# Performance work log

Measured on AMD Instinct MI355X. Metric: run time of the kernel, lower is better.

The kernel has to match this reference:

```python
import jax, jax.numpy as jnp
import numpy as np
import math

DIM = 1024
NUMHEADS = 16
HEAD_DIM = DIM // NUMHEADS
B, N = 4, 1024


def setup_inputs() -> dict:
    key = jax.random.key(0)
    ks = jax.random.split(key, 12)
    x = jax.random.normal(ks[0], (B, N, DIM), dtype=jnp.float32)
    decaymask = jax.random.uniform(ks[1], (NUMHEADS, N, N), dtype=jnp.float32)
    s = 1.0 / math.sqrt(DIM)
    wq = jax.random.normal(ks[2], (DIM, DIM), dtype=jnp.float32) * s
    bq = jnp.zeros((DIM,), dtype=jnp.float32)
    wk = jax.random.normal(ks[3], (DIM, DIM), dtype=jnp.float32) * s
    bk = jnp.zeros((DIM,), dtype=jnp.float32)
    wv = jax.random.normal(ks[4], (DIM, DIM), dtype=jnp.float32) * s
    bv = jnp.zeros((DIM,), dtype=jnp.float32)
    wo = jax.random.normal(ks[5], (DIM, DIM), dtype=jnp.float32) * s
    bo = jnp.zeros((DIM,), dtype=jnp.float32)
    return {"x": x, "decaymask": decaymask, "wq": wq, "bq": bq, "wk": wk,
            "bk": bk, "wv": wv, "bv": bv, "wo": wo, "bo": bo}


def reference(x, decaymask, wq, bq, wk, bk, wv, bv, wo, bo):
    Bx, Nx, D = x.shape
    # projections (torch Linear: x @ W^T + b)
    q = x @ wq.T + bq
    k = x @ wk.T + bk
    v = x @ wv.T + bv
    # [B, H, N, Hd]
    q = q.reshape(Bx, Nx, NUMHEADS, HEAD_DIM).transpose(0, 2, 1, 3)
    k = k.reshape(Bx, Nx, NUMHEADS, HEAD_DIM).transpose(0, 2, 1, 3)
    v = v.reshape(Bx, Nx, NUMHEADS, HEAD_DIM).transpose(0, 2, 1, 3)
    scores = jnp.einsum('bhqd,bhkd->bhqk', q, k) / math.sqrt(HEAD_DIM)
    scores = scores * decaymask[None]  # multiplicative decay mask before softmax
    attn = jax.nn.softmax(scores, axis=-1)
    out = jnp.einsum('bhqk,bhkd->bhqd', attn, v)
    out = out.transpose(0, 2, 1, 3).reshape(Bx, Nx, D)
    return out @ wo.T + bo
```

## Files before the change

kernel.cpp:

```cpp
#include <hip/hip_runtime.h>
#include <hip/hip_bf16.h>
#include <math.h>

typedef __bf16 bf16;
typedef __bf16 bf16x8 __attribute__((ext_vector_type(8)));
typedef __bf16 bf16x4 __attribute__((ext_vector_type(4)));
typedef float f32x4 __attribute__((ext_vector_type(4)));
typedef unsigned short u16;
typedef u16 u16x8 __attribute__((ext_vector_type(8)));

#define SEQ 1024
#define DIMSZ 1024
#define NHEADS 16
#define HEADDIM 64
#define BATCH 4
#define MTOK (BATCH * SEQ)

#define QSCALE 0.180336880f

typedef __attribute__((address_space(1))) const unsigned char gas_u8;
typedef __attribute__((address_space(3))) unsigned char las_u8;
__device__ __forceinline__ void gload16(const void* g, void* l) {
    __builtin_amdgcn_global_load_lds((const gas_u8*)g, (las_u8*)l, 16, 0, 0);
}

__device__ __forceinline__ void cvt_store(const float4 v, bf16* dst, int e0, float scale) {
    int row = e0 >> 10, col = e0 & 1023;
    int col2 = (col & ~63) | (col & 7) | (((((col >> 3) & 7) ^ (row & 7))) << 3);
    bf16x4 o;
    o[0] = (bf16)(v.x * scale);
    o[1] = (bf16)(v.y * scale);
    o[2] = (bf16)(v.z * scale);
    o[3] = (bf16)(v.w * scale);
    *reinterpret_cast<bf16x4*>(&dst[(size_t)row * 1024 + col2]) = o;
}

__global__ void cvt_all(const float4* __restrict__ x,
                        const float4* __restrict__ wq, const float4* __restrict__ wk,
                        const float4* __restrict__ wv, const float4* __restrict__ wo,
                        bf16* __restrict__ xb, bf16* __restrict__ wqkvb,
                        bf16* __restrict__ wob) {
    int i = blockIdx.x * blockDim.x + threadIdx.x;
    if (i < 1048576) {
        cvt_store(x[i], xb, i << 2, 1.f);
    } else {
        int li = i - 1048576;
        int mat = li >> 18, lj = li & 262143;
        const float4* s = (mat == 0) ? wq : (mat == 1) ? wk : (mat == 2) ? wv : wo;
        bf16* d = (mat < 3) ? (wqkvb + (size_t)mat * 1024 * 1024) : wob;
        cvt_store(s[lj], d, lj << 2, (mat == 0) ? QSCALE : 1.f);
    }
}

__device__ __forceinline__ bf16x8 fragswz(const bf16* base, int row, int kb) {
    return *reinterpret_cast<const bf16x8*>(
        reinterpret_cast<const char*>(base) + row * 128 + (kb ^ ((row & 7) << 4)));
}

#define LDT 72
__device__ __forceinline__ bf16x8 ldsfrag72(const bf16* base, int row0, int k0, int lane) {
    return *reinterpret_cast<const bf16x8*>(base + (row0 + (lane & 15)) * LDT + k0 + ((lane >> 4) << 3));
}

template <int WN, int OUT_F32>
__global__ __launch_bounds__(256) void gemm_glds(
    const bf16* __restrict__ A, const bf16* __restrict__ Bm,
    const float* __restrict__ b0, const float* __restrict__ b1, const float* __restrict__ b2,
    float s0, void* __restrict__ Cv, int M, int N, int K)
{
    __shared__ __align__(16) bf16 As[128 * 64];
    __shared__ __align__(16) bf16 Bs[WN * 32 * 64];

    const int BN = WN * 32;
    const int nbn = N / BN;
    const int wrk = (blockIdx.x & 7) * ((int)gridDim.x >> 3) + (blockIdx.x >> 3);
    const int bm = wrk / nbn, bn = wrk % nbn;
    const int m0 = bm << 7, n0 = bn * BN;
    const int tid = threadIdx.x, lane = tid & 63, wid = tid >> 6;
    const int wr = wid >> 1, wc = wid & 1;
    const int lq = lane & 15, g = lane >> 4;

    f32x4 acc[4][WN];
    #pragma unroll
    for (int m = 0; m < 4; ++m)
        #pragma unroll
        for (int n = 0; n < WN; ++n)
            acc[m][n] = (f32x4){0.f, 0.f, 0.f, 0.f};

    for (int kt = 0; kt < K; kt += 64) {
        #pragma unroll
        for (int i = 0; i < 4; ++i) {
            int rb = wid * 32 + i * 8;
            gload16(&A[(size_t)(m0 + rb + (lane >> 3)) * K + kt + ((lane & 7) << 3)],
                    &As[rb * 64]);
        }
        #pragma unroll
        for (int i = 0; i < WN; ++i) {
            int rb = wid * (WN * 8) + i * 8;
            gload16(&Bm[(size_t)(n0 + rb + (lane >> 3)) * K + kt + ((lane & 7) << 3)],
                    &Bs[rb * 64]);
        }
        __syncthreads();

        bf16x8 af[4][2], bfr[WN][2];
        #pragma unroll
        for (int m = 0; m < 4; ++m)
            #pragma unroll
            for (int h2 = 0; h2 < 2; ++h2)
                af[m][h2] = fragswz(As, wr * 64 + m * 16 + lq, h2 * 64 + g * 16);
        #pragma unroll
        for (int n = 0; n < WN; ++n)
            #pragma unroll
            for (int h2 = 0; h2 < 2; ++h2)
                bfr[n][h2] = fragswz(Bs, wc * (WN * 16) + n * 16 + lq, h2 * 64 + g * 16);

        #pragma unroll
        for (int m = 0; m < 4; ++m)
            #pragma unroll
            for (int n = 0; n < WN; ++n)
                #pragma unroll
                for (int h2 = 0; h2 < 2; ++h2)
                    acc[m][n] = __builtin_amdgcn_mfma_f32_16x16x32_bf16(
                        af[m][h2], bfr[n][h2], acc[m][n], 0, 0, 0);
        __syncthreads();
    }

    const int seg = n0 >> 10;
    const float* bp = (seg == 0) ? b0 : ((seg == 1) ? b1 : b2);
    const float bsc = (seg == 0) ? s0 : 1.f;

    #pragma unroll
    for (int m = 0; m < 4; ++m) {
        #pragma unroll
        for (int n = 0; n < WN; ++n) {
            int rbase = m0 + wr * 64 + m * 16 + (g << 2);
            int col = n0 + wc * (WN * 16) + n * 16 + lq;
            float bv = bp[col - (seg << 10)] * bsc;
            #pragma unroll
            for (int r = 0; r < 4; ++r) {
                float v = acc[m][n][r] + bv;
                if (OUT_F32)
                    ((float*)Cv)[(size_t)(rbase + r) * N + col] = v;
                else
                    ((bf16*)Cv)[(size_t)(rbase + r) * N + col] = (bf16)v;
            }
        }
    }
}

struct KVRegs { bf16x8 k0, k1; u16x8 v0, v1; };

__device__ __forceinline__ void issue_loads(KVRegs& r, const bf16* qkv, int brow,
                                            int koff, int voff, int tid) {
    const int rK = tid >> 3, o8 = (tid & 7) << 3;
    r.k0 = *reinterpret_cast<const bf16x8*>(&qkv[(size_t)(brow + rK) * 3072 + koff + o8]);
    r.k1 = *reinterpret_cast<const bf16x8*>(&qkv[(size_t)(brow + rK + 32) * 3072 + koff + o8]);
    const int rV = rK << 1;
    r.v0 = *reinterpret_cast<const u16x8*>(&qkv[(size_t)(brow + rV) * 3072 + voff + o8]);
    r.v1 = *reinterpret_cast<const u16x8*>(&qkv[(size_t)(brow + rV + 1) * 3072 + voff + o8]);
}

__device__ __forceinline__ void write_stage(const KVRegs& r, bf16* Kb, bf16* Vb, int tid) {
    const int rK = tid >> 3, o = tid & 7, o8 = o << 3;
    *reinterpret_cast<bf16x8*>(&Kb[rK * LDT + o8]) = r.k0;
    *reinterpret_cast<bf16x8*>(&Kb[(rK + 32) * LDT + o8]) = r.k1;
    const int rV = rK << 1;
    char* vb = reinterpret_cast<char*>(Vb);
    #pragma unroll
    for (int j = 0; j < 8; ++j) {
        int d = o8 + j;
        int byteo = (d * 144 + rV * 2) ^ (o << 4);
        unsigned int w = (unsigned int)r.v0[j] | ((unsigned int)r.v1[j] << 16);
        *reinterpret_cast<unsigned int*>(vb + byteo) = w;
    }
}

__device__ __forceinline__ void compute_stage(
    const bf16* Kb, const bf16* Vb, bf16* Psw,
    const float4 (&mreg)[4], const bf16x8 (&aqb)[2],
    f32x4& lacc, f32x4 (&oacc)[4], int lane)
{
    const int lq = lane & 15, g = lane >> 4;
    f32x4 sacc[4];
    #pragma unroll
    for (int ct = 0; ct < 4; ++ct) sacc[ct] = (f32x4){0.f, 0.f, 0.f, 0.f};
    #pragma unroll
    for (int ct = 0; ct < 4; ++ct)
        #pragma unroll
        for (int h2 = 0; h2 < 2; ++h2)
            sacc[ct] = __builtin_amdgcn_mfma_f32_16x16x32_bf16(
                ldsfrag72(Kb, ct * 16, h2 * 32, lane), aqb[h2], sacc[ct], 0, 0, 0);

    #pragma unroll
    for (int ct = 0; ct < 4; ++ct) {
        float p0 = __builtin_exp2f(sacc[ct][0] * mreg[ct].x);
        float p1 = __builtin_exp2f(sacc[ct][1] * mreg[ct].y);
        float p2 = __builtin_exp2f(sacc[ct][2] * mreg[ct].z);
        float p3 = __builtin_exp2f(sacc[ct][3] * mreg[ct].w);
        lacc[0] += p0; lacc[1] += p1; lacc[2] += p2; lacc[3] += p3;
        bf16x4 pbv;
        pbv[0] = (bf16)p0; pbv[1] = (bf16)p1; pbv[2] = (bf16)p2; pbv[3] = (bf16)p3;
        *reinterpret_cast<bf16x4*>(&Psw[lq * LDT + ct * 16 + (g << 2)]) = pbv;
    }

    const char* vb = reinterpret_cast<const char*>(Vb);
    #pragma unroll
    for (int ot = 0; ot < 4; ++ot) {
        #pragma unroll
        for (int h2 = 0; h2 < 2; ++h2) {
            int d = ot * 16 + lq;
            int byteo = (d * 144 + (h2 * 32 + g * 8) * 2) ^ (((d >> 3) & 7) << 4);
            bf16x8 vf = *reinterpret_cast<const bf16x8*>(vb + byteo);
            bf16x8 pf = *reinterpret_cast<const bf16x8*>(&Psw[lq * LDT + h2 * 32 + g * 8]);
            oacc[ot] = __builtin_amdgcn_mfma_f32_16x16x32_bf16(vf, pf, oacc[ot], 0, 0, 0);
        }
    }
}

__global__ __launch_bounds__(256) void attn_kernel(
    const bf16* __restrict__ qkv, const float* __restrict__ mask, bf16* __restrict__ Og)
{
    __shared__ __align__(16) bf16 Kbuf[2][64 * LDT];
    __shared__ __align__(16) bf16 Vbuf[2][64 * LDT];
    __shared__ __align__(16) bf16 Ps[4][16 * LDT];

    const int bid = blockIdx.x;
    const int xcd = bid & 7, slot = bid >> 3;
    const int pg = xcd * 32 + (slot >> 1);
    const int bp = slot & 1;
    const int h = pg >> 4, qblk = pg & 15;

    const int tid = threadIdx.x, lane = tid & 63, wid = tid >> 6;
    const int lq = lane & 15, g = lane >> 4;
    const int q = (qblk << 6) + wid * 16 + lq;
    const int koff = 1024 + h * HEADDIM, voff = 2048 + h * HEADDIM, qoff = h * HEADDIM;
    const float* mh = mask + (size_t)h * SEQ * SEQ + (size_t)q * SEQ;

    bf16x8 aq[2][2];
    #pragma unroll
    for (int bi = 0; bi < 2; ++bi)
        #pragma unroll
        for (int h2 = 0; h2 < 2; ++h2)
            aq[bi][h2] = *reinterpret_cast<const bf16x8*>(
                &qkv[(size_t)((bp * 2 + bi) * SEQ + q) * 3072 + qoff + h2 * 32 + g * 8]);

    f32x4 lacc[2] = {};
    f32x4 oacc[2][4] = {};

    KVRegs s0, s1;
    issue_loads(s0, qkv, (bp * 2 + 0) * SEQ, koff, voff, tid);
    issue_loads(s1, qkv, (bp * 2 + 1) * SEQ, koff, voff, tid);
    float4 mregA[4], mregB[4];
    #pragma unroll
    for (int ct = 0; ct < 4; ++ct) {
        mregA[ct] = *reinterpret_cast<const float4*>(&mh[ct * 16 + (g << 2)]);
        mregB[ct] = *reinterpret_cast<const float4*>(&mh[64 + ct * 16 + (g << 2)]);
    }
    write_stage(s0, Kbuf[0], Vbuf[0], tid);
    __syncthreads();

    for (int t = 0; t < 16; ++t) {
        if (t < 15) issue_loads(s0, qkv, (bp * 2 + 0) * SEQ + (t + 1) * 64, koff, voff, tid);
        compute_stage(Kbuf[0], Vbuf[0], Ps[wid], mregA, aq[0], lacc[0], oacc[0], lane);
        write_stage(s1, Kbuf[1], Vbuf[1], tid);
        __syncthreads();

        if (t < 15) issue_loads(s1, qkv, (bp * 2 + 1) * SEQ + (t + 1) * 64, koff, voff, tid);
        compute_stage(Kbuf[1], Vbuf[1], Ps[wid], mregA, aq[1], lacc[1], oacc[1], lane);
        #pragma unroll
        for (int ct = 0; ct < 4; ++ct) mregA[ct] = mregB[ct];
        if (t < 14)
            #pragma unroll
            for (int ct = 0; ct < 4; ++ct)
                mregB[ct] = *reinterpret_cast<const float4*>(&mh[(t + 2) * 64 + ct * 16 + (g << 2)]);
        if (t < 15) write_stage(s0, Kbuf[0], Vbuf[0], tid);
        __syncthreads();
    }

    #pragma unroll
    for (int bi = 0; bi < 2; ++bi) {
        float lsum = lacc[bi][0] + lacc[bi][1] + lacc[bi][2] + lacc[bi][3];
        lsum += __shfl_xor(lsum, 16, 64);
        lsum += __shfl_xor(lsum, 32, 64);
        float inv = 1.f / lsum;
        #pragma unroll
        for (int ot = 0; ot < 4; ++ot) {
            bf16x4 o;
            o[0] = (bf16)(oacc[bi][ot][0] * inv);
            o[1] = (bf16)(oacc[bi][ot][1] * inv);
            o[2] = (bf16)(oacc[bi][ot][2] * inv);
            o[3] = (bf16)(oacc[bi][ot][3] * inv);
            int lcol = ot * 16 + (g << 2);
            int chunk = (lcol >> 3) ^ (q & 7);
            int col = h * HEADDIM + (chunk << 3) + (lcol & 7);
            *reinterpret_cast<bf16x4*>(
                &Og[(size_t)((bp * 2 + bi) * SEQ + q) * DIMSZ + col]) = o;
        }
    }
}

extern "C" void kernel_launch(void* const* d_in, const int* in_sizes, int n_in,
                              void* d_out, int out_size, void* d_ws, size_t ws_size,
                              hipStream_t stream) {
    const float* x    = (const float*)d_in[0];
    const float* mask = (const float*)d_in[1];
    const float* wq   = (const float*)d_in[2];
    const float* bq   = (const float*)d_in[3];
    const float* wk   = (const float*)d_in[4];
    const float* bk   = (const float*)d_in[5];
    const float* wv   = (const float*)d_in[6];
    const float* bv   = (const float*)d_in[7];
    const float* wo   = (const float*)d_in[8];
    const float* bo   = (const float*)d_in[9];
    float* out = (float*)d_out;

    char* ws = (char*)d_ws;
    bf16* xb    = (bf16*)ws; ws += (size_t)MTOK * DIMSZ * 2;
    bf16* wqkvb = (bf16*)ws; ws += (size_t)3 * DIMSZ * DIMSZ * 2;
    bf16* wob   = (bf16*)ws; ws += (size_t)DIMSZ * DIMSZ * 2;
    bf16* qkv   = (bf16*)ws; ws += (size_t)MTOK * 3 * DIMSZ * 2;
    bf16* aob   = (bf16*)ws; ws += (size_t)MTOK * DIMSZ * 2;

    cvt_all<<<(2 * 1048576) / 256, 256, 0, stream>>>(
        (const float4*)x, (const float4*)wq, (const float4*)wk,
        (const float4*)wv, (const float4*)wo, xb, wqkvb, wob);

    gemm_glds<4, 0><<<(MTOK / 128) * (3 * DIMSZ / 128), 256, 0, stream>>>(
        xb, wqkvb, bq, bk, bv, QSCALE, qkv, MTOK, 3 * DIMSZ, DIMSZ);

    attn_kernel<<<512, 256, 0, stream>>>(qkv, mask, aob);

    gemm_glds<2, 1><<<(MTOK / 128) * (DIMSZ / 64), 256, 0, stream>>>(
        aob, wob, bo, bo, bo, 1.f, out, MTOK, DIMSZ, DIMSZ);
}
```

Baseline: 113.6 us.

## Double-buffer K/V per batch with one barrier per step and swizzled K tile

The attention loop now keeps separate ping-pong LDS buffers for both batch elements. It writes the next tile and issues global loads two steps ahead before computing, which halves the number of __syncthreads per iteration and lengthens the distance for hiding global latency. The K tile moves from padded 72-stride rows to a 128-byte XOR-swizzled layout read through fragswz, to avoid bank conflicts while using less padding. LDS use grows (about double for K/V), which may reduce occupancy.

```diff
diff --git a/kernel.cpp b/kernel.cpp
--- a/kernel.cpp
+++ b/kernel.cpp
@@ -58,9 +58,6 @@
 }
 
 #define LDT 72
-__device__ __forceinline__ bf16x8 ldsfrag72(const bf16* base, int row0, int k0, int lane) {
-    return *reinterpret_cast<const bf16x8*>(base + (row0 + (lane & 15)) * LDT + k0 + ((lane >> 4) << 3));
-}
 
 template <int WN, int OUT_F32>
 __global__ __launch_bounds__(256) void gemm_glds(
@@ -161,14 +158,16 @@
 }
 
 __device__ __forceinline__ void write_stage(const KVRegs& r, bf16* Kb, bf16* Vb, int tid) {
-    const int rK = tid >> 3, o = tid & 7, o8 = o << 3;
-    *reinterpret_cast<bf16x8*>(&Kb[rK * LDT + o8]) = r.k0;
-    *reinterpret_cast<bf16x8*>(&Kb[(rK + 32) * LDT + o8]) = r.k1;
+    const int rK = tid >> 3, o = tid & 7;
+    char* kb = reinterpret_cast<char*>(Kb);
+    int kx = (o << 4) ^ ((rK & 7) << 4);
+    *reinterpret_cast<bf16x8*>(kb + rK * 128 + kx) = r.k0;
+    *reinterpret_cast<bf16x8*>(kb + (rK + 32) * 128 + kx) = r.k1;
     const int rV = rK << 1;
     char* vb = reinterpret_cast<char*>(Vb);
     #pragma unroll
     for (int j = 0; j < 8; ++j) {
-        int d = o8 + j;
+        int d = (o << 3) + j;
         int byteo = (d * 144 + rV * 2) ^ (o << 4);
         unsigned int w = (unsigned int)r.v0[j] | ((unsigned int)r.v1[j] << 16);
         *reinterpret_cast<unsigned int*>(vb + byteo) = w;
@@ -189,7 +188,7 @@
         #pragma unroll
         for (int h2 = 0; h2 < 2; ++h2)
             sacc[ct] = __builtin_amdgcn_mfma_f32_16x16x32_bf16(
-                ldsfrag72(Kb, ct * 16, h2 * 32, lane), aqb[h2], sacc[ct], 0, 0, 0);
+                fragswz(Kb, ct * 16 + lq, h2 * 64 + g * 16), aqb[h2], sacc[ct], 0, 0, 0);
 
     #pragma unroll
     for (int ct = 0; ct < 4; ++ct) {
@@ -220,8 +219,8 @@
 __global__ __launch_bounds__(256) void attn_kernel(
     const bf16* __restrict__ qkv, const float* __restrict__ mask, bf16* __restrict__ Og)
 {
-    __shared__ __align__(16) bf16 Kbuf[2][64 * LDT];
-    __shared__ __align__(16) bf16 Vbuf[2][64 * LDT];
+    __shared__ __align__(16) bf16 Kbuf[2][2][64 * 64];
+    __shared__ __align__(16) bf16 Vbuf[2][2][64 * LDT];
     __shared__ __align__(16) bf16 Ps[4][16 * LDT];
 
     const int bid = blockIdx.x;
@@ -234,6 +233,7 @@
     const int lq = lane & 15, g = lane >> 4;
     const int q = (qblk << 6) + wid * 16 + lq;
     const int koff = 1024 + h * HEADDIM, voff = 2048 + h * HEADDIM, qoff = h * HEADDIM;
+    const int b0 = bp * 2, b1 = bp * 2 + 1;
     const float* mh = mask + (size_t)h * SEQ * SEQ + (size_t)q * SEQ;
 
     bf16x8 aq[2][2];
@@ -242,38 +242,44 @@
         #pragma unroll
         for (int h2 = 0; h2 < 2; ++h2)
             aq[bi][h2] = *reinterpret_cast<const bf16x8*>(
-                &qkv[(size_t)((bp * 2 + bi) * SEQ + q) * 3072 + qoff + h2 * 32 + g * 8]);
+                &qkv[(size_t)((b0 + bi) * SEQ + q) * 3072 + qoff + h2 * 32 + g * 8]);
 
     f32x4 lacc[2] = {};
     f32x4 oacc[2][4] = {};
 
     KVRegs s0, s1;
-    issue_loads(s0, qkv, (bp * 2 + 0) * SEQ, koff, voff, tid);
-    issue_loads(s1, qkv, (bp * 2 + 1) * SEQ, koff, voff, tid);
-    float4 mregA[4], mregB[4];
+    issue_loads(s0, qkv, b0 * SEQ, koff, voff, tid);
+    issue_loads(s1, qkv, b1 * SEQ, koff, voff, tid);
+    write_stage(s0, Kbuf[0][0], Vbuf[0][0], tid);
+    write_stage(s1, Kbuf[1][0], Vbuf[1][0], tid);
+    issue_loads(s0, qkv, b0 * SEQ + 64, koff, voff, tid);
+    issue_loads(s1, qkv, b1 * SEQ + 64, koff, voff, tid);
+    float4 mcur[4], mnxt[4];
     #pragma unroll
     for (int ct = 0; ct < 4; ++ct) {
-        mregA[ct] = *reinterpret_cast<const float4*>(&mh[ct * 16 + (g << 2)]);
-        mregB[ct] = *reinterpret_cast<const float4*>(&mh[64 + ct * 16 + (g << 2)]);
-    }
-    write_stage(s0, Kbuf[0], Vbuf[0], tid);
+        mcur[ct] = *reinterpret_cast<const float4*>(&mh[ct * 16 + (g << 2)]);
+        mnxt[ct] = *reinterpret_cast<const float4*>(&mh[64 + ct * 16 + (g << 2)]);
+    }
     __syncthreads();
 
     for (int t = 0; t < 16; ++t) {
-        if (t < 15) issue_loads(s0, qkv, (bp * 2 + 0) * SEQ + (t + 1) * 64, koff, voff, tid);
-        compute_stage(Kbuf[0], Vbuf[0], Ps[wid], mregA, aq[0], lacc[0], oacc[0], lane);
-        write_stage(s1, Kbuf[1], Vbuf[1], tid);
-        __syncthreads();
-
-        if (t < 15) issue_loads(s1, qkv, (bp * 2 + 1) * SEQ + (t + 1) * 64, koff, voff, tid);
-        compute_stage(Kbuf[1], Vbuf[1], Ps[wid], mregA, aq[1], lacc[1], oacc[1], lane);
-        #pragma unroll
-        for (int ct = 0; ct < 4; ++ct) mregA[ct] = mregB[ct];
+        int pp = t & 1, np = pp ^ 1;
+        if (t < 15) {
+            write_stage(s0, Kbuf[0][np], Vbuf[0][np], tid);
+            write_stage(s1, Kbuf[1][np], Vbuf[1][np], tid);
+        }
+        if (t < 14) {
+            issue_loads(s0, qkv, b0 * SEQ + (t + 2) * 64, koff, voff, tid);
+            issue_loads(s1, qkv, b1 * SEQ + (t + 2) * 64, koff, voff, tid);
+        }
+        compute_stage(Kbuf[0][pp], Vbuf[0][pp], Ps[wid], mcur, aq[0], lacc[0], oacc[0], lane);
+        compute_stage(Kbuf[1][pp], Vbuf[1][pp], Ps[wid], mcur, aq[1], lacc[1], oacc[1], lane);
+        #pragma unroll
+        for (int ct = 0; ct < 4; ++ct) mcur[ct] = mnxt[ct];
         if (t < 14)
             #pragma unroll
             for (int ct = 0; ct < 4; ++ct)
-                mregB[ct] = *reinterpret_cast<const float4*>(&mh[(t + 2) * 64 + ct * 16 + (g << 2)]);
-        if (t < 15) write_stage(s0, Kbuf[0], Vbuf[0], tid);
+                mnxt[ct] = *reinterpret_cast<const float4*>(&mh[(t + 2) * 64 + ct * 16 + (g << 2)]);
         __syncthreads();
     }
 
@@ -294,7 +300,7 @@
             int chunk = (lcol >> 3) ^ (q & 7);
             int col = h * HEADDIM + (chunk << 3) + (lcol & 7);
             *reinterpret_cast<bf16x4*>(
-                &Og[(size_t)((bp * 2 + bi) * SEQ + q) * DIMSZ + col]) = o;
+                &Og[(size_t)((b0 + bi) * SEQ + q) * DIMSZ + col]) = o;
         }
     }
 }
```

After: 116.1 us. 2.2% more time.
